# Kernel optimization log

Measured on AMD Instinct MI355X. Metric: run time of the kernel, lower is better.

Reference implementation:

```python
import jax, jax.numpy as jnp
import numpy as np

N, D_IN, D_OUT = 2048, 128, 64


def setup_inputs() -> dict:
    key = jax.random.key(0)
    k1, k2, k3, k4 = jax.random.split(key, 4)
    node_features = jax.random.normal(k1, (N, D_IN), dtype=jnp.float32)
    neighbor_mask = jax.random.randint(k2, (N, N), 0, 2) > 0
    W = jax.random.normal(k3, (D_OUT, D_IN), dtype=jnp.float32) * (1.0 / np.sqrt(D_IN))
    a = jax.random.normal(k4, (2 * D_OUT,), dtype=jnp.float32)
    return {"node_features": node_features, "neighbor_mask": neighbor_mask, "W": W, "a": a}


def reference(node_features, neighbor_mask, W, a):
    # h = Linear(node_features): [N, D_OUT]
    h = node_features @ W.T
    d = h.shape[-1]
    # Additive-attention decomposition: einsum('ijn,n->ij', cat[h_i,h_j], a)
    # == (h @ a[:d])_i + (h @ a[d:])_j  -- same math, no NxNx2D tensor.
    s_i = h @ a[:d]  # [N]
    s_j = h @ a[d:]  # [N]
    scores = jax.nn.leaky_relu(s_i[:, None] + s_j[None, :], negative_slope=0.01)  # [N, N]
    neg_inf = jnp.array(-jnp.inf, dtype=scores.dtype)
    scores = jnp.where(neighbor_mask, scores, neg_inf)
    valid = jnp.any(neighbor_mask, axis=1, keepdims=True)  # [N, 1]
    scores = jnp.where(valid, scores, 0.0)
    alpha = jax.nn.softmax(scores, axis=1)
    alpha = jnp.where(neighbor_mask, alpha, 0.0)
    # messages[i, j, :] = alpha[i, j] * h[j]
    messages = alpha[:, :, None] * h[None, :, :]  # [N, N, D_OUT]
    return messages
```

## Files before the change

### kernel.cpp

```cpp
#include <hip/hip_runtime.h>
#include <math.h>

#define GN 2048
#define GD_IN 128
#define GD_OUT 64

typedef float f4 __attribute__((ext_vector_type(4)));

__global__ __launch_bounds__(64) void gat_h_kernel(
    const float* __restrict__ x,
    const float* __restrict__ W,
    const float* __restrict__ a,
    float* __restrict__ h,
    float* __restrict__ s_i,
    float* __restrict__ s_j) {
    __shared__ float wl[GD_OUT * (GD_IN + 1)];
    __shared__ float xl[GD_IN];
    const int i = blockIdx.x;
    const int t = threadIdx.x;

    for (int idx = t; idx < GD_OUT * GD_IN; idx += 64) {
        int o = idx >> 7, k = idx & 127;
        wl[o * (GD_IN + 1) + k] = W[idx];
    }
    xl[t]      = x[i * GD_IN + t];
    xl[t + 64] = x[i * GD_IN + t + 64];
    __syncthreads();

    float acc = 0.f;
    const float* wr = &wl[t * (GD_IN + 1)];
    #pragma unroll
    for (int k = 0; k < GD_IN; ++k) acc = fmaf(xl[k], wr[k], acc);
    h[i * GD_OUT + t] = acc;

    float p1 = acc * a[t];
    float p2 = acc * a[GD_OUT + t];
    #pragma unroll
    for (int off = 32; off; off >>= 1) {
        p1 += __shfl_down(p1, off);
        p2 += __shfl_down(p2, off);
    }
    if (t == 0) { s_i[i] = p1; s_j[i] = p2; }
}

__global__ __launch_bounds__(256) void gat_msg_kernel(
    const int* __restrict__ mask,
    const float* __restrict__ h,
    const float* __restrict__ s_i,
    const float* __restrict__ s_j,
    float* __restrict__ out) {
    __shared__ float sc[GN];
    __shared__ float red[4];
    const int i = blockIdx.x;
    const int t = threadIdx.x;
    const float si = s_i[i];

    float lmax = -INFINITY;
    for (int j = t; j < GN; j += 256) {
        float z = si + s_j[j];
        float s = z > 0.f ? z : 0.01f * z;
        s = mask[(size_t)i * GN + j] ? s : -INFINITY;
        sc[j] = s;
        lmax = fmaxf(lmax, s);
    }
    #pragma unroll
    for (int off = 32; off; off >>= 1) lmax = fmaxf(lmax, __shfl_down(lmax, off));
    if ((t & 63) == 0) red[t >> 6] = lmax;
    __syncthreads();
    float rmax = fmaxf(fmaxf(red[0], red[1]), fmaxf(red[2], red[3]));
    if (rmax == -INFINITY) rmax = 0.f;

    float lsum = 0.f;
    for (int j = t; j < GN; j += 256) {
        float e = __expf(sc[j] - rmax);
        sc[j] = e;
        lsum += e;
    }
    #pragma unroll
    for (int off = 32; off; off >>= 1) lsum += __shfl_down(lsum, off);
    __syncthreads();
    if ((t & 63) == 0) red[t >> 6] = lsum;
    __syncthreads();
    const float ssum = red[0] + red[1] + red[2] + red[3];
    const float inv = ssum > 0.f ? 1.f / ssum : 0.f;

    for (int j = t; j < GN; j += 256) sc[j] *= inv;
    __syncthreads();

    const f4* __restrict__ h4 = reinterpret_cast<const f4*>(h);
    f4* __restrict__ out4 = reinterpret_cast<f4*>(out) + (size_t)i * GN * (GD_OUT / 4);
    const int jl = t >> 4;
    const int o4 = t & 15;
    #pragma unroll 4
    for (int jb = 0; jb < GN; jb += 16) {
        int j = jb + jl;
        float al = sc[j];
        f4 hv = h4[j * (GD_OUT / 4) + o4];
        out4[(size_t)j * (GD_OUT / 4) + o4] = hv * al;
    }
}

extern "C" void kernel_launch(void* const* d_in, const int* in_sizes, int n_in,
                              void* d_out, int out_size, void* d_ws, size_t ws_size,
                              hipStream_t stream) {
    const float* x    = (const float*)d_in[0];
    const int*   mask = (const int*)d_in[1];
    const float* W    = (const float*)d_in[2];
    const float* a    = (const float*)d_in[3];
    float* out = (float*)d_out;

    float* ws  = (float*)d_ws;
    float* h   = ws;
    float* s_i = ws + GN * GD_OUT;
    float* s_j = s_i + GN;

    gat_h_kernel<<<GN, 64, 0, stream>>>(x, W, a, h, s_i, s_j);
    gat_msg_kernel<<<GN, 256, 0, stream>>>(mask, h, s_i, s_j, out);
}
```

Before: 214.6 us.

## Split message write into separate alpha and persistent broadcast-write kernels

Splits the fused softmax-and-write kernel into two. One kernel computes normalized alpha rows and stores them to a 16 MB workspace matrix. A second kernel of 512 blocks holds one h element vector per thread in registers and loops over i, streaming alpha[i,j]*h[j] to the output. This drops the repeated h reads and aims for a simpler, store-bound write loop, at the cost of an extra global round trip for alpha, one more launch, and strided alpha loads.

```diff
diff --git a/kernel.cpp b/kernel.cpp
--- a/kernel.cpp
+++ b/kernel.cpp
@@ -43,12 +43,11 @@
     if (t == 0) { s_i[i] = p1; s_j[i] = p2; }
 }
 
-__global__ __launch_bounds__(256) void gat_msg_kernel(
+__global__ __launch_bounds__(256) void gat_alpha_kernel(
     const int* __restrict__ mask,
-    const float* __restrict__ h,
     const float* __restrict__ s_i,
     const float* __restrict__ s_j,
-    float* __restrict__ out) {
+    float* __restrict__ alphag) {
     __shared__ float sc[GN];
     __shared__ float red[4];
     const int i = blockIdx.x;
@@ -84,19 +83,26 @@
     const float ssum = red[0] + red[1] + red[2] + red[3];
     const float inv = ssum > 0.f ? 1.f / ssum : 0.f;
 
-    for (int j = t; j < GN; j += 256) sc[j] *= inv;
-    __syncthreads();
+    for (int j = t; j < GN; j += 256)
+        alphag[(size_t)i * GN + j] = sc[j] * inv;
+}
 
-    const f4* __restrict__ h4 = reinterpret_cast<const f4*>(h);
-    f4* __restrict__ out4 = reinterpret_cast<f4*>(out) + (size_t)i * GN * (GD_OUT / 4);
-    const int jl = t >> 4;
-    const int o4 = t & 15;
+__global__ __launch_bounds__(256) void gat_write_kernel(
+    const float* __restrict__ alphag,
+    const float* __restrict__ h,
+    f4* __restrict__ out4) {
+    const int gid = blockIdx.x * 256 + threadIdx.x;
+    const int o4 = gid & 15;
+    const int j  = (gid >> 4) & (GN - 1);
+    const int io = gid >> 15;
+    const f4 hv = reinterpret_cast<const f4*>(h)[(j << 4) | o4];
+
+    const float* __restrict__ ap = alphag + (size_t)io * GN + j;
+    f4* __restrict__ op = out4 + ((((size_t)io * GN + j) << 4) | o4);
     #pragma unroll 4
-    for (int jb = 0; jb < GN; jb += 16) {
-        int j = jb + jl;
-        float al = sc[j];
-        f4 hv = h4[j * (GD_OUT / 4) + o4];
-        out4[(size_t)j * (GD_OUT / 4) + o4] = hv * al;
+    for (int it = 0; it < GN / 4; ++it) {
+        float al = ap[(size_t)it * 4 * GN];
+        op[(size_t)it * 4 * GN * 16] = hv * al;
     }
 }
 
@@ -109,11 +115,13 @@
     const float* a    = (const float*)d_in[3];
     float* out = (float*)d_out;
 
-    float* ws  = (float*)d_ws;
-    float* h   = ws;
-    float* s_i = ws + GN * GD_OUT;
-    float* s_j = s_i + GN;
+    float* ws   = (float*)d_ws;
+    float* h    = ws;
+    float* s_i  = ws + GN * GD_OUT;
+    float* s_j  = s_i + GN;
+    float* alphag = s_j + GN;
 
     gat_h_kernel<<<GN, 64, 0, stream>>>(x, W, a, h, s_i, s_j);
-    gat_msg_kernel<<<GN, 256, 0, stream>>>(mask, h, s_i, s_j, out);
+    gat_alpha_kernel<<<GN, 256, 0, stream>>>(mask, s_i, s_j, alphag);
+    gat_write_kernel<<<512, 256, 0, stream>>>(alphag, h, (f4*)out);
 }
```

Result: slower. 255.9 us (+19.2%).
